# Kernel optimization log

Hardware: AMD Instinct MI355X
Metric: run time of the kernel (lower is better)

## Reference

```python
import jax, jax.numpy as jnp
import numpy as np
import math

L = 2; B = 128; CIN = 64; E = 64; H = 8; Wd = 8; NH = 8; MEM = 40
HD = E // NH; HW = H * Wd; THD = HD * HW  # 512
MASK_B = 3.0; NEG = -1e9; EPS = 1e-5


def _conv(x, w, b):
    y = jax.lax.conv_general_dilated(x, w, (1, 1), 'SAME',
                                     dimension_numbers=('NCHW', 'OIHW', 'NCHW'))
    return y + b[None, :, None, None]


def setup_inputs() -> dict:
    key = jax.random.key(0)
    ks = jax.random.split(key, 12)
    f = jax.random.normal
    return {
        'x': f(ks[0], (B, CIN, H, Wd), jnp.float32),
        'h0': f(ks[1], (L, B, E, H, Wd), jnp.float32),
        'c0': f(ks[2], (L, B, E, H, Wd), jnp.float32),
        'k0': f(ks[3], (L, B, NH, MEM, THD), jnp.float32),
        'v0': f(ks[4], (L, B, NH, MEM, THD), jnp.float32),
        'src_mask': jax.random.randint(ks[5], (B, MEM), 0, 2).astype(bool),
        'notdone': jnp.ones((B,), bool),
        'main_w': f(ks[6], (L, 5 * E, CIN + 2 * E, 3, 3), jnp.float32) * 0.05,
        'main_b': jnp.zeros((L, 5 * E), jnp.float32),
        'proj_w': f(ks[7], (L, 3 * E, CIN + E, 3, 3), jnp.float32) * 0.05,
        'proj_b': jnp.zeros((L, 3 * E), jnp.float32),
        'out_w': f(ks[8], (L, E, E, 3, 3), jnp.float32) * 0.05,
        'out_b': jnp.zeros((L, E), jnp.float32),
        'ln_w': jnp.ones((L, E, H, Wd), jnp.float32),
        'ln_b': jnp.zeros((L, E, H, Wd), jnp.float32),
        'pos_w': f(ks[9], (L, MEM, HW * E), jnp.float32) * 0.05,
        'pos_b': f(ks[10], (L, MEM, NH), jnp.float32) * 0.05,
    }


def reference(x, h0, c0, k0, v0, src_mask, notdone,
              main_w, main_b, proj_w, proj_b, out_w, out_b,
              ln_w, ln_b, pos_w, pos_b):
    nd = notdone.astype(x.dtype)[:, None, None, None]
    # rolling attention mask: reset finished episodes, shift left, open last slot
    m = src_mask | (~notdone)[:, None]
    m = jnp.concatenate([m[:, 1:], jnp.zeros((B, 1), bool)], axis=1)
    bias = jnp.where(m, NEG, 0.0).astype(x.dtype)        # (B, MEM)
    bias = bias.at[:, -1].set(MASK_B)
    out = h0[L - 1] * nd
    for n in range(L):
        inp = jnp.concatenate([x, out], axis=1)          # (B, CIN+E, H, W)
        h_cur = h0[n] * nd
        c_cur = c0[n] * nd
        gates = _conv(jnp.concatenate([inp, h_cur], axis=1), main_w[n], main_b[n])
        cc_i, cc_f, cc_o, cc_g, cc_a = jnp.split(gates, 5, axis=1)
        i = jax.nn.sigmoid(cc_i)
        fg = jax.nn.sigmoid(cc_f)
        o = jax.nn.sigmoid(cc_o)
        g = jnp.tanh(cc_g)
        a = jax.nn.sigmoid(cc_a)
        c_next = fg * c_cur + i * g
        # attention over rolling memory (mem_n slots of flattened spatial features)
        kqv = _conv(inp, proj_w[n], proj_b[n]).reshape(B, NH, 3 * HD, HW)
        k = kqv[:, :, :HD].reshape(B, NH, THD)
        q = kqv[:, :, HD:2 * HD].reshape(B, NH, THD) / math.sqrt(THD)
        v = kqv[:, :, 2 * HD:].reshape(B, NH, THD)
        pw = pos_w[n].reshape(MEM, NH, THD).transpose(1, 0, 2)  # (NH, MEM, THD)
        k_cat = jnp.concatenate([k0[n][:, :, 1:], k[:, :, None, :]], axis=2) + pw[None]
        v_cat = jnp.concatenate([v0[n][:, :, 1:], v[:, :, None, :]], axis=2)
        scores = (jnp.einsum('bnd,bnmd->bnm', q, k_cat)
                  + bias[:, None, :] + pos_b[n].T[None])
        attn_w = jax.nn.softmax(scores, axis=-1)
        attn = jnp.einsum('bnm,bnmd->bnd', attn_w, v_cat).reshape(B, E, H, Wd)
        ao = _conv(attn, out_w[n], out_b[n]) + inp[:, :E]
        mu = ao.mean(axis=(1, 2, 3), keepdims=True)
        var = ((ao - mu) ** 2).mean(axis=(1, 2, 3), keepdims=True)
        ao = (ao - mu) * jax.lax.rsqrt(var + EPS) * ln_w[n][None] + ln_b[n][None]
        c_next = c_next + a * jnp.tanh(ao)
        out = o * jnp.tanh(c_next)
    return out
```

## Files before the change

kernel.cpp:

```cpp
#include <hip/hip_runtime.h>
#include <hip/hip_bf16.h>

typedef __hip_bfloat16 bf16;
typedef unsigned short u16;
typedef __attribute__((ext_vector_type(8))) short short8;
typedef __attribute__((ext_vector_type(4))) float f32x4;

#define Bb   128
#define MEMm 40

__device__ __forceinline__ float LD(const void* p, size_t i, int f32) {
    return f32 ? ((const float*)p)[i] : __bfloat162float(((const bf16*)p)[i]);
}
__device__ __forceinline__ int LDB(const void* p, int i, int isbyte) {
    return isbyte ? (int)((const unsigned char*)p)[i] : ((const int*)p)[i];
}
__device__ __forceinline__ void SPLIT(float v, u16& hi, u16& lo) {
    bf16 h = __float2bfloat16(v);
    float r = v - __bfloat162float(h);
    bf16 l = __float2bfloat16(r);
    hi = *(u16*)&h; lo = *(u16*)&l;
}

__global__ void detect_kernel(const void* __restrict__ x,
                              const void* __restrict__ src_mask,
                              const void* __restrict__ notdone,
                              int* __restrict__ flags) {
    __shared__ int s[3];
    const int t = threadIdx.x;
    if (t < 3) s[t] = 0;
    __syncthreads();
    const bf16* xb = (const bf16*)x;
    int bad = 0;
    for (int i = t; i < 4096; i += 256) {
        float v = __bfloat162float(xb[2 * i]);
        if (!(fabsf(v) < 1e4f)) bad = 1;
    }
    if (bad) atomicOr(&s[0], 1);
    int mb = 0;
    const unsigned* mi = (const unsigned*)src_mask;
    for (int i = t; i < 1280; i += 256) if (mi[i] > 1u) mb = 1;
    if (mb) atomicOr(&s[1], 1);
    int nb = 0;
    const unsigned* ni = (const unsigned*)notdone;
    for (int i = t; i < 32; i += 256) if (ni[i] > 1u) nb = 1;
    if (nb) atomicOr(&s[2], 1);
    __syncthreads();
    if (t < 3) flags[t] = s[t];
}

__global__ void bias_kernel(const void* __restrict__ src_mask,
                            const void* __restrict__ notdone,
                            const int* __restrict__ flags,
                            float* __restrict__ biasb) {
    int idx = blockIdx.x * 256 + threadIdx.x;
    if (idx >= Bb * MEMm) return;
    const int mbyte = flags[1], ndbyte = flags[2];
    int b = idx / MEMm, m = idx - b * MEMm;
    float v;
    if (m == MEMm - 1) v = 3.0f;
    else {
        bool masked = (LDB(src_mask, b * MEMm + m + 1, mbyte) != 0) ||
                      (LDB(notdone, b, ndbyte) == 0);
        v = masked ? -1e9f : 0.f;
    }
    biasb[idx] = v;
}

__global__ void init_prevout_kernel(const void* __restrict__ h0,
                                    const void* __restrict__ notdone,
                                    const int* __restrict__ flags,
                                    float* __restrict__ outb, size_t off) {
    int idx = blockIdx.x * 256 + threadIdx.x;
    if (idx >= Bb * 4096) return;
    const int isf32 = flags[0], ndbyte = flags[2];
    int b = idx >> 12;
    float nd = (LDB(notdone, b, ndbyte) != 0) ? 1.f : 0.f;
    outb[idx] = LD(h0, off + idx, isf32) * nd;
}

__global__ void repack_w_kernel(const void* __restrict__ mw,
                                const void* __restrict__ pw,
                                const void* __restrict__ ow,
                                const int* __restrict__ flags,
                                u16* __restrict__ whi, u16* __restrict__ wlo,
                                int layer) {
    int i = blockIdx.x * 256 + threadIdx.x;
    if (i >= 811008) return;
    const int isf32 = flags[0];
    float v;
    if (i < 552960) {
        int tap = i / 61440, r = i - tap * 61440, co = r / 192, ci = r - co * 192;
        v = LD(mw, (size_t)layer * 552960 + ((size_t)co * 192 + ci) * 9 + tap, isf32);
    } else if (i < 774144) {
        int j = i - 552960;
        int tap = j / 24576, r = j - tap * 24576, co = r / 128, ci = r - co * 128;
        v = LD(pw, (size_t)layer * 221184 + ((size_t)co * 128 + ci) * 9 + tap, isf32);
    } else {
        int j = i - 774144;
        int tap = j / 4096, r = j - tap * 4096, co = r / 64, ci = r - co * 64;
        v = LD(ow, (size_t)layer * 36864 + ((size_t)co * 64 + ci) * 9 + tap, isf32);
    }
    u16 h, l; SPLIT(v, h, l);
    whi[i] = h; wlo[i] = l;
}

__global__ __launch_bounds__(256) void build_cin_t_kernel(
    const void* __restrict__ x, const float* __restrict__ prev_out,
    const void* __restrict__ h0, const void* __restrict__ notdone,
    const int* __restrict__ flags,
    u16* __restrict__ cin_hi, u16* __restrict__ cin_lo, size_t hoff) {
    __shared__ float sb[192 * 65];
    const int t = threadIdx.x, b = blockIdx.x;
    const int isf32 = flags[0], ndbyte = flags[2];
    float nd = (LDB(notdone, b, ndbyte) != 0) ? 1.f : 0.f;
    for (int i = t; i < 12288; i += 256) {
        int c = i >> 6, px = i & 63;
        float v;
        if (c < 64)       v = LD(x, (size_t)b * 4096 + i, isf32);
        else if (c < 128) v = prev_out[(size_t)b * 4096 + i - 4096];
        else              v = LD(h0, hoff + (size_t)b * 4096 + i - 8192, isf32) * nd;
        sb[c * 65 + px] = v;
    }
    __syncthreads();
    size_t base = (size_t)b * 12288;
    for (int i = t; i < 12288; i += 256) {
        int px = i / 192, c = i - px * 192;
        float v = sb[c * 65 + px];
        u16 h, l; SPLIT(v, h, l);
        cin_hi[base + i] = h; cin_lo[base + i] = l;
    }
}

struct ConvArgs {
    const u16 *Ahi, *Alo;
    const u16 *WhiA, *WloA, *WhiB, *WloB;
    const void *biasA, *biasB;
    float *OutA, *OutB;
    long long boffA, boffB;
    int Astr, KciA, KciB, CoutA, CoutB, ntA, NT;
};

__global__ __launch_bounds__(256) void conv_mfma_kernel(ConvArgs g,
                                                        const int* __restrict__ flags) {
    __shared__ __align__(16) u16 Alds[4][2][2600];
    __shared__ __align__(16) u16 Wlds[2][2][2560];
    const int t = threadIdx.x, w = t >> 6, lane = t & 63;
    const int bx = blockIdx.x;
    const int nt = bx % g.NT, mblk = bx / g.NT;
    const bool isA = (nt < g.ntA);
    const u16* Whi = isA ? g.WhiA : g.WhiB;
    const u16* Wlo = isA ? g.WloA : g.WloB;
    const int Kci  = isA ? g.KciA : g.KciB;
    const int CoutT= isA ? g.CoutA : g.CoutB;
    float* Out     = isA ? g.OutA : g.OutB;
    const void* bias = isA ? g.biasA : g.biasB;
    const long long boff = isA ? g.boffA : g.boffB;
    const int n0 = (isA ? nt : nt - g.ntA) * 64;
    const int b = mblk * 4 + w;
    const int NITER = (Kci >> 5) * 9;
    const int isf32 = flags[0];

    if (lane < 40) { Alds[w][0][2560 + lane] = 0; Alds[w][1][2560 + lane] = 0; }

    f32x4 acc[4][4];
#pragma unroll
    for (int i = 0; i < 4; ++i)
#pragma unroll
        for (int j = 0; j < 4; ++j) { f32x4 z = {0.f, 0.f, 0.f, 0.f}; acc[i][j] = z; }

    const int co_l = t >> 2, jj = t & 3;
    uint4 hv, lv;
    auto issueW = [&](int it) {
        int kc = it / 9, tap = it - kc * 9;
        size_t o = ((size_t)(tap * CoutT + n0 + co_l)) * Kci + kc * 32 + jj * 8;
        hv = *(const uint4*)(Whi + o);
        lv = *(const uint4*)(Wlo + o);
    };

    issueW(0);
    for (int it = 0; it < NITER; ++it) {
        const int kc = it / 9, tap = it - kc * 9;
        const int par = it & 1;
        *(uint4*)&Wlds[par][0][co_l * 40 + jj * 8] = hv;
        *(uint4*)&Wlds[par][1][co_l * 40 + jj * 8] = lv;
        __syncthreads();
        if (it + 1 < NITER) issueW(it + 1);
        if (tap == 0) {
            size_t o = ((size_t)b * 64 + lane) * g.Astr + kc * 32;
            const uint4* sh = (const uint4*)(g.Ahi + o);
            const uint4* sl = (const uint4*)(g.Alo + o);
            uint4 a0 = sh[0], a1 = sh[1], a2 = sh[2], a3 = sh[3];
            uint4 c0 = sl[0], c1 = sl[1], c2 = sl[2], c3 = sl[3];
            *(uint4*)&Alds[w][0][lane * 40 + 0]  = a0;
            *(uint4*)&Alds[w][0][lane * 40 + 8]  = a1;
            *(uint4*)&Alds[w][0][lane * 40 + 16] = a2;
            *(uint4*)&Alds[w][0][lane * 40 + 24] = a3;
            *(uint4*)&Alds[w][1][lane * 40 + 0]  = c0;
            *(uint4*)&Alds[w][1][lane * 40 + 8]  = c1;
            *(uint4*)&Alds[w][1][lane * 40 + 16] = c2;
            *(uint4*)&Alds[w][1][lane * 40 + 24] = c3;
        }
        const int dy = tap / 3 - 1, dx = tap % 3 - 1;
        const int q8 = (lane >> 4) * 8;
        const int ml = lane & 15;
        short8 aH[4], aL[4];
#pragma unroll
        for (int mt = 0; mt < 4; ++mt) {
            int px = mt * 16 + ml;
            int yy = (px >> 3) + dy, xx = (px & 7) + dx;
            int row = ((unsigned)yy < 8u && (unsigned)xx < 8u) ? yy * 8 + xx : 64;
            int o = row * 40 + q8;
            aH[mt] = *(const short8*)&Alds[w][0][o];
            aL[mt] = *(const short8*)&Alds[w][1][o];
        }
#pragma unroll
        for (int nn = 0; nn < 4; ++nn) {
            int o = (nn * 16 + ml) * 40 + q8;
            short8 bH = *(const short8*)&Wlds[par][0][o];
            short8 bL = *(const short8*)&Wlds[par][1][o];
#pragma unroll
            for (int mt = 0; mt < 4; ++mt) {
                acc[mt][nn] = __builtin_amdgcn_mfma_f32_16x16x32_bf16(aH[mt], bH, acc[mt][nn], 0, 0, 0);
                acc[mt][nn] = __builtin_amdgcn_mfma_f32_16x16x32_bf16(aH[mt], bL, acc[mt][nn], 0, 0, 0);
                acc[mt][nn] = __builtin_amdgcn_mfma_f32_16x16x32_bf16(aL[mt], bH, acc[mt][nn], 0, 0, 0);
            }
        }
    }
    const int q = lane >> 4, ml = lane & 15;
#pragma unroll
    for (int nn = 0; nn < 4; ++nn) {
        int co = n0 + nn * 16 + ml;
        float bv = LD(bias, (size_t)boff + co, isf32);
#pragma unroll
        for (int mt = 0; mt < 4; ++mt) {
            f32x4 v = acc[mt][nn];
            v[0] += bv; v[1] += bv; v[2] += bv; v[3] += bv;
            *(f32x4*)&Out[((size_t)b * CoutT + co) * 64 + mt * 16 + q * 4] = v;
        }
    }
}

__global__ __launch_bounds__(256) void attn_kernel(
    const float* __restrict__ kqv,
    const void* __restrict__ k0,
    const void* __restrict__ v0,
    const void* __restrict__ pw,
    const void* __restrict__ pb,
    const float* __restrict__ biasb,
    const int* __restrict__ flags,
    u16* __restrict__ ahi, u16* __restrict__ alo,
    size_t kvoff, size_t pwoff, size_t pboff) {
    __shared__ float q[512], kl[512], vl[512], sc[40], wexp[40];
    const int t = threadIdx.x;
    const int isf32 = flags[0];
    const int b = blockIdx.x >> 3, h = blockIdx.x & 7;
    const size_t kqb = (size_t)b * 192 * 64;
    for (int d = t; d < 512; d += 256) {
        int hd = d >> 6, ss = d & 63;
        q[d]  = kqv[kqb + (h * 24 + 8 + hd) * 64 + ss] * 0.044194173824159216f;
        kl[d] = kqv[kqb + (h * 24 + 0 + hd) * 64 + ss];
        vl[d] = kqv[kqb + (h * 24 + 16 + hd) * 64 + ss];
    }
    __syncthreads();
    const int wid = t >> 6, lane = t & 63;
    const size_t kvbase = kvoff + ((size_t)(b * 8 + h)) * (size_t)(40 * 512);
    for (int m = wid; m < 40; m += 4) {
        float p = 0.f;
        if (isf32) {
#pragma unroll
            for (int i = 0; i < 8; ++i) {
                int d = lane + 64 * i;
                float kc = (m < 39) ? ((const float*)k0)[kvbase + (size_t)(m + 1) * 512 + d] : kl[d];
                kc += ((const float*)pw)[pwoff + (size_t)m * 4096 + h * 512 + d];
                p += q[d] * kc;
            }
        } else {
#pragma unroll
            for (int i = 0; i < 8; ++i) {
                int d = lane + 64 * i;
                float kc = (m < 39) ? __bfloat162float(((const bf16*)k0)[kvbase + (size_t)(m + 1) * 512 + d]) : kl[d];
                kc += __bfloat162float(((const bf16*)pw)[pwoff + (size_t)m * 4096 + h * 512 + d]);
                p += q[d] * kc;
            }
        }
#pragma unroll
        for (int off = 32; off > 0; off >>= 1) p += __shfl_down(p, off, 64);
        if (lane == 0)
            sc[m] = p + biasb[b * 40 + m] + LD(pb, pboff + m * 8 + h, isf32);
    }
    __syncthreads();
    float mx = -1e30f;
    for (int m = 0; m < 40; ++m) mx = fmaxf(mx, sc[m]);
    if (t < 40) wexp[t] = __expf(sc[t] - mx);
    __syncthreads();
    float sum = 0.f;
    for (int m = 0; m < 40; ++m) sum += wexp[m];
    float rs = 1.f / sum;
    for (int d = t; d < 512; d += 256) {
        float acc = 0.f;
        if (isf32) {
            for (int m = 0; m < 39; ++m)
                acc += wexp[m] * ((const float*)v0)[kvbase + (size_t)(m + 1) * 512 + d];
        } else {
            for (int m = 0; m < 39; ++m)
                acc += wexp[m] * __bfloat162float(((const bf16*)v0)[kvbase + (size_t)(m + 1) * 512 + d]);
        }
        acc += wexp[39] * vl[d];
        acc *= rs;
        int ch = h * 8 + (d >> 6), px = d & 63;
        u16 hh, ll; SPLIT(acc, hh, ll);
        size_t o = (size_t)b * 4096 + px * 64 + ch;
        ahi[o] = hh; alo[o] = ll;
    }
}

__global__ __launch_bounds__(256) void ln_final_kernel(
    const float* __restrict__ convo,
    const void* __restrict__ x,
    const float* __restrict__ gates,
    const void* __restrict__ c0,
    const void* __restrict__ notdone,
    const void* __restrict__ lnw,
    const void* __restrict__ lnb,
    const int* __restrict__ flags,
    float* __restrict__ out_buf,
    void* __restrict__ dout, int write_out,
    size_t coff, size_t lnoff) {
    __shared__ float red[8];
    __shared__ float stats[2];
    const int t = threadIdx.x, b = blockIdx.x;
    const int isf32 = flags[0], ndbyte = flags[2];
    const size_t base = (size_t)b * 4096;
    float v[16];
    float sum = 0.f, sumsq = 0.f;
#pragma unroll
    for (int k = 0; k < 16; ++k) {
        int i = t + 256 * k;
        float val = convo[base + i] + LD(x, base + i, isf32);
        v[k] = val; sum += val; sumsq += val * val;
    }
#pragma unroll
    for (int off = 32; off > 0; off >>= 1) {
        sum   += __shfl_down(sum, off, 64);
        sumsq += __shfl_down(sumsq, off, 64);
    }
    const int wid = t >> 6, lane = t & 63;
    if (lane == 0) { red[wid] = sum; red[4 + wid] = sumsq; }
    __syncthreads();
    if (t == 0) {
        float ts = red[0] + red[1] + red[2] + red[3];
        float tq = red[4] + red[5] + red[6] + red[7];
        float mu = ts * (1.f / 4096.f);
        float var = tq * (1.f / 4096.f) - mu * mu;
        stats[0] = mu; stats[1] = rsqrtf(fmaxf(var, 0.f) + 1e-5f);
    }
    __syncthreads();
    float mu = stats[0], rstd = stats[1];
    float nd = (LDB(notdone, b, ndbyte) != 0) ? 1.f : 0.f;
    const size_t gbase = (size_t)b * 320 * 64;
#pragma unroll
    for (int k = 0; k < 16; ++k) {
        int i = t + 256 * k;
        int c = i >> 6, s = i & 63;
        float aon = (v[k] - mu) * rstd * LD(lnw, lnoff + i, isf32) + LD(lnb, lnoff + i, isf32);
        float gi = gates[gbase + (size_t)(c      ) * 64 + s];
        float gf = gates[gbase + (size_t)(c +  64) * 64 + s];
        float go = gates[gbase + (size_t)(c + 128) * 64 + s];
        float gg = gates[gbase + (size_t)(c + 192) * 64 + s];
        float ga = gates[gbase + (size_t)(c + 256) * 64 + s];
        gi = 1.f / (1.f + __expf(-gi));
        gf = 1.f / (1.f + __expf(-gf));
        go = 1.f / (1.f + __expf(-go));
        gg = tanhf(gg);
        ga = 1.f / (1.f + __expf(-ga));
        float cc = LD(c0, coff + base + i, isf32) * nd;
        float cn = gf * cc + gi * gg + ga * tanhf(aon);
        float o  = go * tanhf(cn);
        out_buf[base + i] = o;
        if (write_out) {
            if (isf32) ((float*)dout)[base + i] = o;
            else       ((bf16*)dout)[base + i] = __float2bfloat16(o);
        }
    }
}

extern "C" void kernel_launch(void* const* d_in, const int* in_sizes, int n_in,
                              void* d_out, int out_size, void* d_ws, size_t ws_size,
                              hipStream_t stream) {
    const void* x      = d_in[0];
    const void* h0     = d_in[1];
    const void* c0     = d_in[2];
    const void* k0     = d_in[3];
    const void* v0     = d_in[4];
    const void* src_mask = d_in[5];
    const void* notdone  = d_in[6];
    const void* main_w = d_in[7];
    const void* main_b = d_in[8];
    const void* proj_w = d_in[9];
    const void* proj_b = d_in[10];
    const void* out_w  = d_in[11];
    const void* out_b  = d_in[12];
    const void* ln_w   = d_in[13];
    const void* ln_b   = d_in[14];
    const void* pos_w  = d_in[15];
    const void* pos_b  = d_in[16];

    float* wsf = (float*)d_ws;
    int*   flags    = (int*)d_ws;
    float* bias_buf = wsf + 8;
    float* out_buf  = wsf + 8192;
    float* gates_buf= wsf + 532480;
    float* kqv_buf  = wsf + 3153920;
    u16* cin_hi     = (u16*)(wsf + 4726784);
    u16* cin_lo     = (u16*)(wsf + 5513216);
    float* convo_buf= wsf + 4726784;
    u16* attn_hi    = (u16*)(wsf + 5513216);
    u16* attn_lo    = (u16*)(wsf + 5775360);
    u16* wr_hi      = (u16*)(wsf + 6299648);
    u16* wr_lo      = (u16*)(wsf + 6705152);

    detect_kernel<<<1, 256, 0, stream>>>(x, src_mask, notdone, flags);
    bias_kernel<<<20, 256, 0, stream>>>(src_mask, notdone, flags, bias_buf);
    init_prevout_kernel<<<2048, 256, 0, stream>>>(h0, notdone, flags, out_buf,
                                                  (size_t)524288);
    for (int n = 0; n < 2; ++n) {
        repack_w_kernel<<<3168, 256, 0, stream>>>(main_w, proj_w, out_w, flags,
                                                  wr_hi, wr_lo, n);
        build_cin_t_kernel<<<128, 256, 0, stream>>>(x, out_buf, h0, notdone, flags,
                                                    cin_hi, cin_lo, (size_t)n * 524288);
        ConvArgs ga;
        ga.Ahi = cin_hi; ga.Alo = cin_lo; ga.Astr = 192;
        ga.WhiA = wr_hi;          ga.WloA = wr_lo;          ga.KciA = 192; ga.CoutA = 320;
        ga.WhiB = wr_hi + 552960; ga.WloB = wr_lo + 552960; ga.KciB = 128; ga.CoutB = 192;
        ga.biasA = main_b; ga.boffA = (long long)n * 320; ga.OutA = gates_buf;
        ga.biasB = proj_b; ga.boffB = (long long)n * 192; ga.OutB = kqv_buf;
        ga.ntA = 5; ga.NT = 8;
        conv_mfma_kernel<<<256, 256, 0, stream>>>(ga, flags);

        attn_kernel<<<1024, 256, 0, stream>>>(
            kqv_buf, k0, v0, pos_w, pos_b, bias_buf, flags, attn_hi, attn_lo,
            (size_t)n * 20971520, (size_t)n * 163840, (size_t)n * 320);

        ConvArgs oa;
        oa.Ahi = attn_hi; oa.Alo = attn_lo; oa.Astr = 64;
        oa.WhiA = wr_hi + 774144; oa.WloA = wr_lo + 774144; oa.KciA = 64; oa.CoutA = 64;
        oa.WhiB = oa.WhiA; oa.WloB = oa.WloA; oa.KciB = 64; oa.CoutB = 64;
        oa.biasA = out_b; oa.boffA = (long long)n * 64; oa.OutA = convo_buf;
        oa.biasB = out_b; oa.boffB = (long long)n * 64; oa.OutB = convo_buf;
        oa.ntA = 1; oa.NT = 1;
        conv_mfma_kernel<<<32, 256, 0, stream>>>(oa, flags);

        ln_final_kernel<<<128, 256, 0, stream>>>(
            convo_buf, x, gates_buf, c0, notdone, ln_w, ln_b, flags,
            out_buf, d_out, (n == 1) ? 1 : 0,
            (size_t)n * 524288, (size_t)n * 4096);
    }
}
```

Before: 636.6 us.

## Vectorize attention K/V loads, split V reduction across waves, batch weight repack

```diff
diff --git a/kernel.cpp b/kernel.cpp
--- a/kernel.cpp
+++ b/kernel.cpp
@@ -11,6 +11,10 @@
 
 __device__ __forceinline__ float LD(const void* p, size_t i, int f32) {
     return f32 ? ((const float*)p)[i] : __bfloat162float(((const bf16*)p)[i]);
+}
+__device__ __forceinline__ float S2F(short s) {
+    u16 u = (u16)s;
+    return __bfloat162float(*(bf16*)&u);
 }
 __device__ __forceinline__ int LDB(const void* p, int i, int isbyte) {
     return isbyte ? (int)((const unsigned char*)p)[i] : ((const int*)p)[i];
@@ -72,22 +76,36 @@
                                     const int* __restrict__ flags,
                                     float* __restrict__ outb, size_t off) {
     int idx = blockIdx.x * 256 + threadIdx.x;
-    if (idx >= Bb * 4096) return;
+    if (idx >= Bb * 512) return;
     const int isf32 = flags[0], ndbyte = flags[2];
-    int b = idx >> 12;
+    int b = idx >> 9;
     float nd = (LDB(notdone, b, ndbyte) != 0) ? 1.f : 0.f;
-    outb[idx] = LD(h0, off + idx, isf32) * nd;
+    size_t e = (size_t)idx * 8;
+    float v[8];
+    if (isf32) {
+        const float* hp = (const float*)h0 + off + e;
+        f32x4 a = *(const f32x4*)hp, c = *(const f32x4*)(hp + 4);
+#pragma unroll
+        for (int j = 0; j < 4; ++j) { v[j] = a[j]; v[4 + j] = c[j]; }
+    } else {
+        short8 s = *(const short8*)((const bf16*)h0 + off + e);
+#pragma unroll
+        for (int j = 0; j < 8; ++j) v[j] = S2F(s[j]);
+    }
+#pragma unroll
+    for (int j = 0; j < 8; ++j) outb[e + j] = v[j] * nd;
 }
 
 __global__ void repack_w_kernel(const void* __restrict__ mw,
                                 const void* __restrict__ pw,
                                 const void* __restrict__ ow,
                                 const int* __restrict__ flags,
-                                u16* __restrict__ whi, u16* __restrict__ wlo,
-                                int layer) {
-    int i = blockIdx.x * 256 + threadIdx.x;
-    if (i >= 811008) return;
+                                u16* __restrict__ whi, u16* __restrict__ wlo) {
+    int gi = blockIdx.x * 256 + threadIdx.x;
+    if (gi >= 1622016) return;
     const int isf32 = flags[0];
+    int layer = (gi >= 811008) ? 1 : 0;
+    int i = gi - layer * 811008;
     float v;
     if (i < 552960) {
         int tap = i / 61440, r = i - tap * 61440, co = r / 192, ci = r - co * 192;
@@ -102,7 +120,7 @@
         v = LD(ow, (size_t)layer * 36864 + ((size_t)co * 64 + ci) * 9 + tap, isf32);
     }
     u16 h, l; SPLIT(v, h, l);
-    whi[i] = h; wlo[i] = l;
+    whi[gi] = h; wlo[gi] = l;
 }
 
 __global__ __launch_bounds__(256) void build_cin_t_kernel(
@@ -251,45 +269,64 @@
     const int* __restrict__ flags,
     u16* __restrict__ ahi, u16* __restrict__ alo,
     size_t kvoff, size_t pwoff, size_t pboff) {
-    __shared__ float q[512], kl[512], vl[512], sc[40], wexp[40];
+    __shared__ float qv[512], kl[512], vl[512], sc[40], wexp[40];
+    __shared__ float accbuf[4][512];
     const int t = threadIdx.x;
     const int isf32 = flags[0];
     const int b = blockIdx.x >> 3, h = blockIdx.x & 7;
     const size_t kqb = (size_t)b * 192 * 64;
     for (int d = t; d < 512; d += 256) {
         int hd = d >> 6, ss = d & 63;
-        q[d]  = kqv[kqb + (h * 24 + 8 + hd) * 64 + ss] * 0.044194173824159216f;
+        qv[d] = kqv[kqb + (h * 24 + 8 + hd) * 64 + ss] * 0.044194173824159216f;
         kl[d] = kqv[kqb + (h * 24 + 0 + hd) * 64 + ss];
         vl[d] = kqv[kqb + (h * 24 + 16 + hd) * 64 + ss];
     }
     __syncthreads();
     const int wid = t >> 6, lane = t & 63;
+    const int d0 = lane * 8;
     const size_t kvbase = kvoff + ((size_t)(b * 8 + h)) * (size_t)(40 * 512);
+
+    float q8[8];
+#pragma unroll
+    for (int j = 0; j < 8; ++j) q8[j] = qv[d0 + j];
+
     for (int m = wid; m < 40; m += 4) {
-        float p = 0.f;
-        if (isf32) {
-#pragma unroll
-            for (int i = 0; i < 8; ++i) {
-                int d = lane + 64 * i;
-                float kc = (m < 39) ? ((const float*)k0)[kvbase + (size_t)(m + 1) * 512 + d] : kl[d];
-                kc += ((const float*)pw)[pwoff + (size_t)m * 4096 + h * 512 + d];
-                p += q[d] * kc;
+        float kc[8];
+        if (m < 39) {
+            if (isf32) {
+                const float* kp = (const float*)k0 + kvbase + (size_t)(m + 1) * 512 + d0;
+                f32x4 a = *(const f32x4*)kp, c = *(const f32x4*)(kp + 4);
+#pragma unroll
+                for (int j = 0; j < 4; ++j) { kc[j] = a[j]; kc[4 + j] = c[j]; }
+            } else {
+                short8 s = *(const short8*)((const bf16*)k0 + kvbase + (size_t)(m + 1) * 512 + d0);
+#pragma unroll
+                for (int j = 0; j < 8; ++j) kc[j] = S2F(s[j]);
             }
         } else {
 #pragma unroll
-            for (int i = 0; i < 8; ++i) {
-                int d = lane + 64 * i;
-                float kc = (m < 39) ? __bfloat162float(((const bf16*)k0)[kvbase + (size_t)(m + 1) * 512 + d]) : kl[d];
-                kc += __bfloat162float(((const bf16*)pw)[pwoff + (size_t)m * 4096 + h * 512 + d]);
-                p += q[d] * kc;
-            }
-        }
+            for (int j = 0; j < 8; ++j) kc[j] = kl[d0 + j];
+        }
+        if (isf32) {
+            const float* pp = (const float*)pw + pwoff + (size_t)m * 4096 + h * 512 + d0;
+            f32x4 a = *(const f32x4*)pp, c = *(const f32x4*)(pp + 4);
+#pragma unroll
+            for (int j = 0; j < 4; ++j) { kc[j] += a[j]; kc[4 + j] += c[j]; }
+        } else {
+            short8 s = *(const short8*)((const bf16*)pw + pwoff + (size_t)m * 4096 + h * 512 + d0);
+#pragma unroll
+            for (int j = 0; j < 8; ++j) kc[j] += S2F(s[j]);
+        }
+        float p = 0.f;
+#pragma unroll
+        for (int j = 0; j < 8; ++j) p += q8[j] * kc[j];
 #pragma unroll
         for (int off = 32; off > 0; off >>= 1) p += __shfl_down(p, off, 64);
         if (lane == 0)
             sc[m] = p + biasb[b * 40 + m] + LD(pb, pboff + m * 8 + h, isf32);
     }
     __syncthreads();
+
     float mx = -1e30f;
     for (int m = 0; m < 40; ++m) mx = fmaxf(mx, sc[m]);
     if (t < 40) wexp[t] = __expf(sc[t] - mx);
@@ -297,16 +334,34 @@
     float sum = 0.f;
     for (int m = 0; m < 40; ++m) sum += wexp[m];
     float rs = 1.f / sum;
+
+    float acc8[8];
+#pragma unroll
+    for (int j = 0; j < 8; ++j) acc8[j] = 0.f;
+    for (int m = wid; m < 40; m += 4) {
+        float wgt = wexp[m];
+        if (m < 39) {
+            if (isf32) {
+                const float* vp = (const float*)v0 + kvbase + (size_t)(m + 1) * 512 + d0;
+                f32x4 a = *(const f32x4*)vp, c = *(const f32x4*)(vp + 4);
+#pragma unroll
+                for (int j = 0; j < 4; ++j) { acc8[j] += wgt * a[j]; acc8[4 + j] += wgt * c[j]; }
+            } else {
+                short8 s = *(const short8*)((const bf16*)v0 + kvbase + (size_t)(m + 1) * 512 + d0);
+#pragma unroll
+                for (int j = 0; j < 8; ++j) acc8[j] += wgt * S2F(s[j]);
+            }
+        } else {
+#pragma unroll
+            for (int j = 0; j < 8; ++j) acc8[j] += wgt * vl[d0 + j];
+        }
+    }
+#pragma unroll
+    for (int j = 0; j < 8; ++j) accbuf[wid][d0 + j] = acc8[j];
+    __syncthreads();
+
     for (int d = t; d < 512; d += 256) {
-        float acc = 0.f;
-        if (isf32) {
-            for (int m = 0; m < 39; ++m)
-                acc += wexp[m] * ((const float*)v0)[kvbase + (size_t)(m + 1) * 512 + d];
-        } else {
-            for (int m = 0; m < 39; ++m)
-                acc += wexp[m] * __bfloat162float(((const bf16*)v0)[kvbase + (size_t)(m + 1) * 512 + d]);
-        }
-        acc += wexp[39] * vl[d];
+        float acc = (accbuf[0][d] + accbuf[1][d]) + (accbuf[2][d] + accbuf[3][d]);
         acc *= rs;
         int ch = h * 8 + (d >> 6), px = d & 63;
         u16 hh, ll; SPLIT(acc, hh, ll);
@@ -418,21 +473,22 @@
     u16* attn_hi    = (u16*)(wsf + 5513216);
     u16* attn_lo    = (u16*)(wsf + 5775360);
     u16* wr_hi      = (u16*)(wsf + 6299648);
-    u16* wr_lo      = (u16*)(wsf + 6705152);
+    u16* wr_lo      = (u16*)(wsf + 7110656);
 
     detect_kernel<<<1, 256, 0, stream>>>(x, src_mask, notdone, flags);
     bias_kernel<<<20, 256, 0, stream>>>(src_mask, notdone, flags, bias_buf);
-    init_prevout_kernel<<<2048, 256, 0, stream>>>(h0, notdone, flags, out_buf,
-                                                  (size_t)524288);
+    init_prevout_kernel<<<256, 256, 0, stream>>>(h0, notdone, flags, out_buf,
+                                                 (size_t)524288);
+    repack_w_kernel<<<6336, 256, 0, stream>>>(main_w, proj_w, out_w, flags,
+                                              wr_hi, wr_lo);
     for (int n = 0; n < 2; ++n) {
-        repack_w_kernel<<<3168, 256, 0, stream>>>(main_w, proj_w, out_w, flags,
-                                                  wr_hi, wr_lo, n);
+        const size_t wb = (size_t)n * 811008;
         build_cin_t_kernel<<<128, 256, 0, stream>>>(x, out_buf, h0, notdone, flags,
                                                     cin_hi, cin_lo, (size_t)n * 524288);
         ConvArgs ga;
         ga.Ahi = cin_hi; ga.Alo = cin_lo; ga.Astr = 192;
-        ga.WhiA = wr_hi;          ga.WloA = wr_lo;          ga.KciA = 192; ga.CoutA = 320;
-        ga.WhiB = wr_hi + 552960; ga.WloB = wr_lo + 552960; ga.KciB = 128; ga.CoutB = 192;
+        ga.WhiA = wr_hi + wb;          ga.WloA = wr_lo + wb;          ga.KciA = 192; ga.CoutA = 320;
+        ga.WhiB = wr_hi + wb + 552960; ga.WloB = wr_lo + wb + 552960; ga.KciB = 128; ga.CoutB = 192;
         ga.biasA = main_b; ga.boffA = (long long)n * 320; ga.OutA = gates_buf;
         ga.biasB = proj_b; ga.boffB = (long long)n * 192; ga.OutB = kqv_buf;
         ga.ntA = 5; ga.NT = 8;
@@ -444,7 +500,7 @@
 
         ConvArgs oa;
         oa.Ahi = attn_hi; oa.Alo = attn_lo; oa.Astr = 64;
-        oa.WhiA = wr_hi + 774144; oa.WloA = wr_lo + 774144; oa.KciA = 64; oa.CoutA = 64;
+        oa.WhiA = wr_hi + wb + 774144; oa.WloA = wr_lo + wb + 774144; oa.KciA = 64; oa.CoutA = 64;
         oa.WhiB = oa.WhiA; oa.WloB = oa.WloA; oa.KciB = 64; oa.CoutB = 64;
         oa.biasA = out_b; oa.boffA = (long long)n * 64; oa.OutA = convo_buf;
         oa.biasB = out_b; oa.boffB = (long long)n * 64; oa.OutB = convo_buf;
```

Result: no change. 640.6 us (+0.6%).
